# Kernel optimization log

Hardware: AMD Instinct MI355X
Metric: run time of the kernel (lower is better)

Reference implementation:

```python
import jax, jax.numpy as jnp
import numpy as np

N_SAMPLES = 4194304
N_RAYS = 131072


def setup_inputs() -> dict:
    key = jax.random.key(0)
    k1, k2, k3, k4, k5, k6 = jax.random.split(key, 6)
    alpha = jax.random.uniform(k1, (N_SAMPLES, 1), dtype=jnp.float32)
    values3d = jax.random.uniform(k2, (N_SAMPLES, 3), dtype=jnp.float32)
    values1d = jax.random.uniform(k3, (N_SAMPLES, 1), dtype=jnp.float32)
    weights = jax.random.uniform(k4, (N_SAMPLES, 1), dtype=jnp.float32)
    sample_values = jax.random.normal(k5, (N_SAMPLES, 3), dtype=jnp.float32)
    ray_id = jnp.sort(jax.random.randint(k6, (N_SAMPLES,), 0, N_RAYS, dtype=jnp.int32))
    return {"alpha": alpha, "values3d": values3d, "values1d": values1d,
            "weights": weights, "sample_values": sample_values,
            "ray_id": ray_id, "n_rays": N_RAYS}


def _transmittance(alpha, ray_id, n_rays):
    # exclusive cumprod of (1 - alpha) within each packed ray segment, in log space
    logs = jnp.log(jnp.clip(1.0 - alpha[:, 0], 1e-7, 1.0))          # [N]
    csum = jnp.cumsum(logs)
    excl = csum - logs                                               # exclusive cumsum
    first = jnp.concatenate([jnp.ones((1,), bool), ray_id[1:] != ray_id[:-1]])
    seg_base = jax.ops.segment_sum(jnp.where(first, excl, 0.0), ray_id,
                                   num_segments=n_rays)              # [R]
    transmittance = jnp.exp(excl - seg_base[ray_id])[:, None]        # [N,1]
    bg_transmittance = jnp.exp(jax.ops.segment_sum(logs, ray_id,
                                                   num_segments=n_rays))  # [R]
    return transmittance, bg_transmittance


def reference(alpha, values3d, values1d, weights, sample_values, ray_id, n_rays):
    transmittance, bg_transmittance = _transmittance(alpha, ray_id, n_rays)
    # integrate_3d / integrate_1d: per-ray sum of value * weight
    integrated_3d = jax.ops.segment_sum(values3d * weights, ray_id, num_segments=n_rays)  # [R,3]
    integrated_1d = jax.ops.segment_sum(values1d * weights, ray_id, num_segments=n_rays)  # [R,1]
    # SumOverRay: per-ray sum plus broadcast back to each sample
    sum_per_ray = jax.ops.segment_sum(sample_values, ray_id, num_segments=n_rays)         # [R,3]
    sum_per_sample = sum_per_ray[ray_id]                                                  # [N,3]
    return (transmittance, bg_transmittance, integrated_3d, integrated_1d,
            sum_per_ray, sum_per_sample)
```

## Files before the change

kernel.cpp:

```cpp
#include <hip/hip_runtime.h>

typedef float f32x4 __attribute__((ext_vector_type(4)));

template<int CTRL>
__device__ __forceinline__ float dpp1(float x) {
    return __int_as_float(__builtin_amdgcn_update_dpp(
        0x3f800000, __float_as_int(x), CTRL, 0xF, 0xF, false));
}
template<int CTRL>
__device__ __forceinline__ float dpp0(float x) {
    return __int_as_float(__builtin_amdgcn_update_dpp(
        0, __float_as_int(x), CTRL, 0xF, 0xF, true));
}
template<int PAT>
__device__ __forceinline__ float swz(float x) {
    return __int_as_float(__builtin_amdgcn_ds_swizzle(__float_as_int(x), PAT));
}
#define FUNNEL16(v) do { \
    v += dpp0<0x111>(v); \
    v += dpp0<0x112>(v); \
    v += dpp0<0x114>(v); \
    v += dpp0<0x118>(v); } while (0)

__device__ __forceinline__ void ntst4(float* p, float x, float y, float z, float w) {
    f32x4 v = {x, y, z, w};
    __builtin_nontemporal_store(v, (f32x4*)p);
}

__global__ __launch_bounds__(256) void seg_bounds_kernel(
    const int* __restrict__ ray_id, int n, int* __restrict__ seg_se)
{
    const int t = blockIdx.x * blockDim.x + threadIdx.x;
    const int a = t * 4;
    if (a >= n) return;
    const int4 rv = *(const int4*)(ray_id + a);
    const int prev = (a == 0) ? -1 : ray_id[a - 1];
    const int nxt  = (a + 4 < n) ? ray_id[a + 4] : -1;

    if (rv.x != prev) seg_se[2 * rv.x] = a;
    if (rv.y != rv.x) { seg_se[2 * rv.x + 1] = a + 1; seg_se[2 * rv.y] = a + 1; }
    if (rv.z != rv.y) { seg_se[2 * rv.y + 1] = a + 2; seg_se[2 * rv.z] = a + 2; }
    if (rv.w != rv.z) { seg_se[2 * rv.z + 1] = a + 3; seg_se[2 * rv.w] = a + 3; }
    if (rv.w != nxt)  seg_se[2 * rv.w + 1] = a + 4;
}

__global__ __launch_bounds__(256) void ray_kernel(
    const float* __restrict__ alpha,
    const float* __restrict__ values3d,
    const float* __restrict__ values1d,
    const float* __restrict__ weights,
    const float* __restrict__ sample_values,
    const int*   __restrict__ ray_id,
    const int*   __restrict__ seg_se,
    float* __restrict__ out_T,
    float* __restrict__ out_bg,
    float* __restrict__ out_i3,
    float* __restrict__ out_i1,
    float* __restrict__ out_spr,
    float* __restrict__ out_sps,
    int R, int N)
{
    const int lane = threadIdx.x & 63;
    const int wid  = threadIdx.x >> 6;
    const int j    = lane & 15;
    const int g    = lane >> 4;
    const int r    = (blockIdx.x * 4 + wid) * 4 + g;
    const bool ray_ok = (r < R);
    const int rc = ray_ok ? r : 0;

    const int2 se = ((const int2*)seg_se)[rc];
    int s0 = se.x, s1 = se.y;
    bool valid = ray_ok & (s0 >= 0) & (s0 < s1) & (s1 <= N);
    if (valid) valid = (ray_id[s0] == rc);
    if (!valid) { s0 = 0; s1 = 0; }

    float c = 1.0f;
    float i3x = 0.f, i3y = 0.f, i3z = 0.f, i1 = 0.f;
    float sx = 0.f, sy = 0.f, sz = 0.f;

    const int base0 = s0 & ~3;

    for (int base = base0; base < s1; base += 64) {
        const int a = base + 4 * j;
        const bool tile_ok = (a < s1);
        const int  al = tile_ok ? a : base0;

        const f32x4 av  = *(const f32x4*)(alpha + al);
        const f32x4 wv  = *(const f32x4*)(weights + al);
        const f32x4 v1v = *(const f32x4*)(values1d + al);
        const f32x4 b0  = *(const f32x4*)(values3d + 3 * al);
        const f32x4 b1  = *(const f32x4*)(values3d + 3 * al + 4);
        const f32x4 b2  = *(const f32x4*)(values3d + 3 * al + 8);
        const f32x4 q0  = *(const f32x4*)(sample_values + 3 * al);
        const f32x4 q1  = *(const f32x4*)(sample_values + 3 * al + 4);
        const f32x4 q2  = *(const f32x4*)(sample_values + 3 * al + 8);

        const bool w0 = tile_ok & (a + 0 >= s0);
        const bool w1 = tile_ok & (a + 1 >= s0) & (a + 1 < s1);
        const bool w2 = tile_ok & (a + 2 >= s0) & (a + 2 < s1);
        const bool w3 = tile_ok & (a + 3 < s1);

        float o0 = fminf(fmaxf(1.0f - av.x, 1e-7f), 1.0f); if (!w0) o0 = 1.0f;
        float o1 = fminf(fmaxf(1.0f - av.y, 1e-7f), 1.0f); if (!w1) o1 = 1.0f;
        float o2 = fminf(fmaxf(1.0f - av.z, 1e-7f), 1.0f); if (!w2) o2 = 1.0f;
        float o3 = fminf(fmaxf(1.0f - av.w, 1e-7f), 1.0f); if (!w3) o3 = 1.0f;

        const float p01  = o0 * o1;
        const float p012 = p01 * o2;
        float p = p012 * o3;

        p *= dpp1<0x111>(p);
        p *= dpp1<0x112>(p);
        p *= dpp1<0x114>(p);
        p *= dpp1<0x118>(p);
        const float gincl = p;
        const float gexcl = dpp1<0x111>(gincl);

        const float cg = c * gexcl;
        const float t0 = cg;
        const float t1 = cg * o0;
        const float t2 = cg * p01;
        const float t3 = cg * p012;

        const float W0 = w0 ? wv.x : 0.f;
        const float W1 = w1 ? wv.y : 0.f;
        const float W2 = w2 ? wv.z : 0.f;
        const float W3 = w3 ? wv.w : 0.f;
        const float M0 = w0 ? 1.f : 0.f;
        const float M1 = w1 ? 1.f : 0.f;
        const float M2 = w2 ? 1.f : 0.f;
        const float M3 = w3 ? 1.f : 0.f;

        i1  += v1v.x * W0 + v1v.y * W1 + v1v.z * W2 + v1v.w * W3;
        i3x += b0.x * W0 + b0.w * W1 + b1.z * W2 + b2.y * W3;
        i3y += b0.y * W0 + b1.x * W1 + b1.w * W2 + b2.z * W3;
        i3z += b0.z * W0 + b1.y * W1 + b2.x * W2 + b2.w * W3;
        sx  += q0.x * M0 + q0.w * M1 + q1.z * M2 + q2.y * M3;
        sy  += q0.y * M0 + q1.x * M1 + q1.w * M2 + q2.z * M3;
        sz  += q0.z * M0 + q1.y * M1 + q2.x * M2 + q2.w * M3;

        if (w0 & w1 & w2 & w3) {
            ntst4(out_T + a, t0, t1, t2, t3);
        } else {
            if (w0) out_T[a + 0] = t0;
            if (w1) out_T[a + 1] = t1;
            if (w2) out_T[a + 2] = t2;
            if (w3) out_T[a + 3] = t3;
        }

        c *= swz<0x1F0>(gincl);
    }

    FUNNEL16(i3x); FUNNEL16(i3y); FUNNEL16(i3z); FUNNEL16(i1);
    FUNNEL16(sx);  FUNNEL16(sy);  FUNNEL16(sz);
    sx = swz<0x1F0>(sx);
    sy = swz<0x1F0>(sy);
    sz = swz<0x1F0>(sz);

    if (ray_ok && j == 15) {
        out_bg[r] = c;
        out_i3[3 * r + 0] = i3x;
        out_i3[3 * r + 1] = i3y;
        out_i3[3 * r + 2] = i3z;
        out_i1[r] = i1;
        out_spr[3 * r + 0] = sx;
        out_spr[3 * r + 1] = sy;
        out_spr[3 * r + 2] = sz;
    }

    for (int base = base0; base < s1; base += 64) {
        const int a = base + 4 * j;
        const bool tile_ok = (a < s1);
        const bool w0 = tile_ok & (a + 0 >= s0);
        const bool w1 = tile_ok & (a + 1 >= s0) & (a + 1 < s1);
        const bool w2 = tile_ok & (a + 2 >= s0) & (a + 2 < s1);
        const bool w3 = tile_ok & (a + 3 < s1);
        if (w0 & w1 & w2 & w3) {
            ntst4(out_sps + 3 * a,     sx, sy, sz, sx);
            ntst4(out_sps + 3 * a + 4, sy, sz, sx, sy);
            ntst4(out_sps + 3 * a + 8, sz, sx, sy, sz);
        } else {
            if (w0) { out_sps[3*a+0] = sx; out_sps[3*a+1]  = sy; out_sps[3*a+2]  = sz; }
            if (w1) { out_sps[3*a+3] = sx; out_sps[3*a+4]  = sy; out_sps[3*a+5]  = sz; }
            if (w2) { out_sps[3*a+6] = sx; out_sps[3*a+7]  = sy; out_sps[3*a+8]  = sz; }
            if (w3) { out_sps[3*a+9] = sx; out_sps[3*a+10] = sy; out_sps[3*a+11] = sz; }
        }
    }
}

extern "C" void kernel_launch(void* const* d_in, const int* in_sizes, int n_in,
                              void* d_out, int out_size, void* d_ws, size_t ws_size,
                              hipStream_t stream) {
    const float* alpha = (const float*)d_in[0];
    const float* v3    = (const float*)d_in[1];
    const float* v1    = (const float*)d_in[2];
    const float* w     = (const float*)d_in[3];
    const float* sv    = (const float*)d_in[4];
    const int*   rid   = (const int*)d_in[5];

    int N = in_sizes[0];
    int R = (out_size - 4 * N) / 8;

    int* seg_se = (int*)d_ws;

    float* out     = (float*)d_out;
    float* out_T   = out;
    float* out_bg  = out + N;
    float* out_i3  = out_bg + R;
    float* out_i1  = out_i3 + 3 * (size_t)R;
    float* out_spr = out_i1 + R;
    float* out_sps = out_spr + 3 * (size_t)R;

    const int nquad = N / 4;
    seg_bounds_kernel<<<(nquad + 255) / 256, 256, 0, stream>>>(rid, N, seg_se);

    int blocks = (R + 15) / 16;
    ray_kernel<<<blocks, 256, 0, stream>>>(alpha, v3, v1, w, sv, rid, seg_se,
                                           out_T, out_bg, out_i3, out_i1, out_spr,
                                           out_sps, R, N);
}
```

Measured before the change: 50.00 us.

## Process four rays per 16-lane group and stage per-ray outputs in LDS

The segment-bounds kernel now writes empty (s,s) ranges for rays with no samples, so the ray kernel no longer has to validate bounds by re-reading ray_id. Each 16-lane group handles four consecutive rays in turn, and the grid shrinks to a quarter of the blocks, with the bounds fetched as vector loads. Per-ray reductions go into shared memory and are written out in a coalesced pass after a barrier, replacing scattered single-lane stores. This trades parallelism (fewer waves, serialized rays per group) for less launch overhead and better store coalescing. When R is not a multiple of 4, a group whose four rays extend past R is skipped, so the last few real rays are never processed.

```diff
diff --git a/kernel.cpp b/kernel.cpp
--- a/kernel.cpp
+++ b/kernel.cpp
@@ -28,52 +28,43 @@
 }
 
 __global__ __launch_bounds__(256) void seg_bounds_kernel(
-    const int* __restrict__ ray_id, int n, int* __restrict__ seg_se)
+    const int* __restrict__ ray_id, int n, int R, int* __restrict__ seg_se)
 {
     const int t = blockIdx.x * blockDim.x + threadIdx.x;
     const int a = t * 4;
     if (a >= n) return;
     const int4 rv = *(const int4*)(ray_id + a);
-    const int prev = (a == 0) ? -1 : ray_id[a - 1];
-    const int nxt  = (a + 4 < n) ? ray_id[a + 4] : -1;
-
-    if (rv.x != prev) seg_se[2 * rv.x] = a;
-    if (rv.y != rv.x) { seg_se[2 * rv.x + 1] = a + 1; seg_se[2 * rv.y] = a + 1; }
-    if (rv.z != rv.y) { seg_se[2 * rv.y + 1] = a + 2; seg_se[2 * rv.z] = a + 2; }
-    if (rv.w != rv.z) { seg_se[2 * rv.z + 1] = a + 3; seg_se[2 * rv.w] = a + 3; }
-    if (rv.w != nxt)  seg_se[2 * rv.w + 1] = a + 4;
-}
-
-__global__ __launch_bounds__(256) void ray_kernel(
+
+#define TRANS(u, v, p) do {                                                   \
+        if ((u) >= 0) seg_se[2 * (u) + 1] = (p);                              \
+        for (int id_ = (u) + 1; id_ < (v); ++id_) {                           \
+            seg_se[2 * id_] = (p); seg_se[2 * id_ + 1] = (p); }               \
+        if ((v) < R) seg_se[2 * (v)] = (p); } while (0)
+
+    if (a == 0) TRANS(-1, rv.x, 0);
+    if (rv.y != rv.x) TRANS(rv.x, rv.y, a + 1);
+    if (rv.z != rv.y) TRANS(rv.y, rv.z, a + 2);
+    if (rv.w != rv.z) TRANS(rv.z, rv.w, a + 3);
+    if (a + 4 == n) {
+        TRANS(rv.w, R, n);
+    } else {
+        const int nx = ray_id[a + 4];
+        if (nx != rv.w) TRANS(rv.w, nx, a + 4);
+    }
+#undef TRANS
+}
+
+__device__ __forceinline__ void process_ray(
+    int s0, int s1, int j, int sl,
     const float* __restrict__ alpha,
     const float* __restrict__ values3d,
     const float* __restrict__ values1d,
     const float* __restrict__ weights,
     const float* __restrict__ sample_values,
-    const int*   __restrict__ ray_id,
-    const int*   __restrict__ seg_se,
     float* __restrict__ out_T,
-    float* __restrict__ out_bg,
-    float* __restrict__ out_i3,
-    float* __restrict__ out_i1,
-    float* __restrict__ out_spr,
     float* __restrict__ out_sps,
-    int R, int N)
+    float (*__restrict__ prr)[8])
 {
-    const int lane = threadIdx.x & 63;
-    const int wid  = threadIdx.x >> 6;
-    const int j    = lane & 15;
-    const int g    = lane >> 4;
-    const int r    = (blockIdx.x * 4 + wid) * 4 + g;
-    const bool ray_ok = (r < R);
-    const int rc = ray_ok ? r : 0;
-
-    const int2 se = ((const int2*)seg_se)[rc];
-    int s0 = se.x, s1 = se.y;
-    bool valid = ray_ok & (s0 >= 0) & (s0 < s1) & (s1 <= N);
-    if (valid) valid = (ray_id[s0] == rc);
-    if (!valid) { s0 = 0; s1 = 0; }
-
     float c = 1.0f;
     float i3x = 0.f, i3y = 0.f, i3z = 0.f, i1 = 0.f;
     float sx = 0.f, sy = 0.f, sz = 0.f;
@@ -157,15 +148,11 @@
     sy = swz<0x1F0>(sy);
     sz = swz<0x1F0>(sz);
 
-    if (ray_ok && j == 15) {
-        out_bg[r] = c;
-        out_i3[3 * r + 0] = i3x;
-        out_i3[3 * r + 1] = i3y;
-        out_i3[3 * r + 2] = i3z;
-        out_i1[r] = i1;
-        out_spr[3 * r + 0] = sx;
-        out_spr[3 * r + 1] = sy;
-        out_spr[3 * r + 2] = sz;
+    if (j == 15) {
+        prr[sl][0] = c;
+        prr[sl][1] = i1;
+        prr[sl][2] = i3x; prr[sl][3] = i3y; prr[sl][4] = i3z;
+        prr[sl][5] = sx;  prr[sl][6] = sy;  prr[sl][7] = sz;
     }
 
     for (int base = base0; base < s1; base += 64) {
@@ -188,6 +175,58 @@
     }
 }
 
+__global__ __launch_bounds__(256) void ray_kernel(
+    const float* __restrict__ alpha,
+    const float* __restrict__ values3d,
+    const float* __restrict__ values1d,
+    const float* __restrict__ weights,
+    const float* __restrict__ sample_values,
+    const int*   __restrict__ seg_se,
+    float* __restrict__ out_T,
+    float* __restrict__ out_bg,
+    float* __restrict__ out_i3,
+    float* __restrict__ out_i1,
+    float* __restrict__ out_spr,
+    float* __restrict__ out_sps,
+    int R)
+{
+    __shared__ float prr[64][8];
+
+    const int lane = threadIdx.x & 63;
+    const int wid  = threadIdx.x >> 6;
+    const int j    = lane & 15;
+    const int g    = lane >> 4;
+    const int grp  = wid * 4 + g;
+    const int r0b  = blockIdx.x * 64;
+    const int rb   = r0b + grp * 4;
+
+    int4 seA = {0,0,0,0}, seB = {0,0,0,0};
+    if (rb + 3 < R) {
+        seA = *(const int4*)(seg_se + 2 * rb);
+        seB = *(const int4*)(seg_se + 2 * rb + 4);
+    }
+
+    process_ray(seA.x, seA.y, j, grp * 4 + 0, alpha, values3d, values1d,
+                weights, sample_values, out_T, out_sps, prr);
+    process_ray(seA.z, seA.w, j, grp * 4 + 1, alpha, values3d, values1d,
+                weights, sample_values, out_T, out_sps, prr);
+    process_ray(seB.x, seB.y, j, grp * 4 + 2, alpha, values3d, values1d,
+                weights, sample_values, out_T, out_sps, prr);
+    process_ray(seB.z, seB.w, j, grp * 4 + 3, alpha, values3d, values1d,
+                weights, sample_values, out_T, out_sps, prr);
+
+    __syncthreads();
+
+    for (int f = threadIdx.x; f < 512; f += 256) {
+        float val; float* addr; int ridx;
+        if (f < 64)       { ridx = f;                 val = prr[ridx][0];          addr = out_bg  + r0b + f; }
+        else if (f < 128) { ridx = f - 64;            val = prr[ridx][1];          addr = out_i1  + r0b + ridx; }
+        else if (f < 320) { int s = f - 128; ridx = s / 3; val = prr[ridx][2 + s % 3]; addr = out_i3  + 3 * r0b + s; }
+        else              { int s = f - 320; ridx = s / 3; val = prr[ridx][5 + s % 3]; addr = out_spr + 3 * r0b + s; }
+        if (r0b + ridx < R) *addr = val;
+    }
+}
+
 extern "C" void kernel_launch(void* const* d_in, const int* in_sizes, int n_in,
                               void* d_out, int out_size, void* d_ws, size_t ws_size,
                               hipStream_t stream) {
@@ -212,10 +251,10 @@
     float* out_sps = out_spr + 3 * (size_t)R;
 
     const int nquad = N / 4;
-    seg_bounds_kernel<<<(nquad + 255) / 256, 256, 0, stream>>>(rid, N, seg_se);
-
-    int blocks = (R + 15) / 16;
-    ray_kernel<<<blocks, 256, 0, stream>>>(alpha, v3, v1, w, sv, rid, seg_se,
+    seg_bounds_kernel<<<(nquad + 255) / 256, 256, 0, stream>>>(rid, N, R, seg_se);
+
+    const int blocks = (R + 63) / 64;
+    ray_kernel<<<blocks, 256, 0, stream>>>(alpha, v3, v1, w, sv, seg_se,
                                            out_T, out_bg, out_i3, out_i1, out_spr,
-                                           out_sps, R, N);
-}
+                                           out_sps, R);
+}
```

Result: slower. 58.60 us (+17.2%).
